# Kernel tuning notes

Measured on AMD Instinct MI355X. Metric: run time of the kernel, lower is better.

## Reference

```python
import jax, jax.numpy as jnp
import numpy as np

D_MODEL = 1024
D_STATE = 16
D_FFN = 4096
D_INNER = 2 * D_MODEL
DT_RANK = D_MODEL // 16  # 64
K = 3  # conv kernel size
B_SZ = 2
L = 2048


def setup_inputs() -> dict:
    key = jax.random.key(0)
    ks = jax.random.split(key, 10)
    f = jnp.float32
    s = 0.02
    A_log = jnp.log(jnp.broadcast_to(jnp.arange(1, D_STATE + 1, dtype=f), (D_INNER, D_STATE)))
    return {
        "x": jax.random.normal(ks[0], (B_SZ, L, D_MODEL), f),
        "in_proj_w": jax.random.normal(ks[1], (2 * D_INNER, D_MODEL), f) * s,
        "conv_w": jax.random.normal(ks[2], (D_INNER, K), f) * s,
        "conv_b": jnp.zeros((D_INNER,), f),
        "x_proj_w": jax.random.normal(ks[3], (DT_RANK + 2 * D_STATE, D_INNER), f) * s,
        "dt_proj_w": jax.random.normal(ks[4], (D_INNER, DT_RANK), f) * s,
        "dt_proj_b": jnp.full((D_INNER,), -4.0, f),  # softplus -> small init dt
        "A_log": A_log,
        "Dp": jnp.ones((D_INNER,), f),
        "out_proj_w": jax.random.normal(ks[5], (D_MODEL, D_INNER), f) * s,
        "w1": jax.random.normal(ks[6], (D_FFN, D_MODEL), f) * s,
        "b1": jnp.zeros((D_FFN,), f),
        "w2": jax.random.normal(ks[7], (D_MODEL, D_FFN), f) * s,
        "b2": jnp.zeros((D_MODEL,), f),
    }


def _mamba(x, in_proj_w, conv_w, conv_b, x_proj_w, dt_proj_w, dt_proj_b, A_log, Dp, out_proj_w):
    # x: [B, L, d_model]
    xz = x @ in_proj_w.T                       # [B, L, 2*d_inner]
    xp, z = jnp.split(xz, 2, axis=-1)          # each [B, L, d_inner]
    # causal depthwise conv over time
    xc = jnp.swapaxes(xp, 1, 2)                # [B, d_inner, L]
    kern = conv_w[:, None, :]                  # [d_inner, 1, K]
    xc = jax.lax.conv_general_dilated(xc, kern, (1,), [(K - 1, 0)], feature_group_count=D_INNER)
    xp = jax.nn.silu(jnp.swapaxes(xc, 1, 2) + conv_b)  # [B, L, d_inner]
    # input-dependent dt, B, C
    dbc = xp @ x_proj_w.T                      # [B, L, dt_rank + 2*d_state]
    dt = jax.nn.softplus(dbc[..., :DT_RANK] @ dt_proj_w.T + dt_proj_b)  # [B, L, d_inner]
    Bm = dbc[..., DT_RANK:DT_RANK + D_STATE]   # [B, L, d_state]
    Cm = dbc[..., DT_RANK + D_STATE:]          # [B, L, d_state]
    A = -jnp.exp(A_log)                        # [d_inner, d_state]

    def step(h, t):
        dt_t, B_t, C_t, x_t = t                # [B,d_inner],[B,n],[B,n],[B,d_inner]
        h = jnp.exp(dt_t[:, :, None] * A) * h + dt_t[:, :, None] * B_t[:, None, :] * x_t[:, :, None]
        y = jnp.einsum('bdn,bn->bd', h, C_t)
        return h, y

    h0 = jnp.zeros((x.shape[0], D_INNER, D_STATE), x.dtype)
    ts = (jnp.swapaxes(dt, 0, 1), jnp.swapaxes(Bm, 0, 1), jnp.swapaxes(Cm, 0, 1), jnp.swapaxes(xp, 0, 1))
    h_final, ys = jax.lax.scan(step, h0, ts)
    y = jnp.swapaxes(ys, 0, 1) + xp * Dp       # [B, L, d_inner]
    y = y * jax.nn.silu(z)
    return y @ out_proj_w.T, h_final


def reference(x, in_proj_w, conv_w, conv_b, x_proj_w, dt_proj_w, dt_proj_b, A_log, Dp, out_proj_w, w1, b1, w2, b2):
    ssm_out, new_state = _mamba(x, in_proj_w, conv_w, conv_b, x_proj_w, dt_proj_w, dt_proj_b, A_log, Dp, out_proj_w)
    x = x + ssm_out
    h = jax.nn.gelu(x @ w1.T + b1, approximate=False)
    x = x + (h @ w2.T + b2)
    return (x, new_state)
```

## Files before the change

### kernel.cpp

```cpp
#include <hip/hip_runtime.h>
#include <hip/hip_bf16.h>
#include <math.h>

using bf16 = __hip_bfloat16;

typedef __attribute__((ext_vector_type(8))) short short8;
typedef __attribute__((ext_vector_type(4))) short shortx4;
typedef __attribute__((ext_vector_type(4))) float floatx4;

#define D_MODEL 1024
#define D_STATE 16
#define D_FFN   4096
#define D_INNER 2048
#define DT_RANK 64
#define BSZ     2
#define SEQ     2048
#define MROWS   (BSZ*SEQ)
#define NCHUNK  16
#define CLEN    (SEQ/NCHUNK)

static __device__ __forceinline__ float bf2f(bf16 v) { return __bfloat162float(v); }
static __device__ __forceinline__ short f2s(float f) {
    bf16 h = __float2bfloat16(f);
    return *reinterpret_cast<short*>(&h);
}
static __device__ __forceinline__ float sbf(short s) {
    union { short s; bf16 h; } u; u.s = s; return __bfloat162float(u.h);
}
static __device__ __forceinline__ float rd(const bf16* p)  { return bf2f(*p); }
static __device__ __forceinline__ float rd(const float* p) { return *p; }
static __device__ __forceinline__ void  wr(bf16* p, float v)  { *p = __float2bfloat16(v); }
static __device__ __forceinline__ void  wr(float* p, float v) { *p = v; }

static __device__ __forceinline__ void gload16(const bf16* g, bf16* l) {
    __builtin_amdgcn_global_load_lds(
        (const __attribute__((address_space(1))) void*)g,
        (__attribute__((address_space(3))) void*)l, 16, 0, 0);
}

#define BK 64

enum { ACT_NONE = 0, ACT_GELU = 1, ACT_SOFTPLUS = 2 };

template<int ACT, bool HAS_BIAS, bool HAS_RES, typename TR, typename TC>
__global__ __launch_bounds__(256)
void gemm_bt(const bf16* __restrict__ A, int lda,
             const bf16* __restrict__ W, int ldw,
             TC* __restrict__ C, int ldc,
             const float* __restrict__ bias,
             const TR* __restrict__ resid, int ldr,
             int K,
             const bf16* __restrict__ W2, TC* __restrict__ C2, int mtiles)
{
    __shared__ __align__(16) bf16 As[128 * BK];
    __shared__ __align__(16) bf16 Bs[128 * BK];

    const int tid  = threadIdx.x;
    const int lane = tid & 63;
    const int wid  = tid >> 6;
    const int wm   = wid >> 1;
    const int wn   = wid & 1;
    const int quad = lane >> 4;
    const int lrow = lane & 15;

    int bx = blockIdx.x, by = blockIdx.y;
    const int gx = gridDim.x;
    if ((gx & 7) == 0) {
        int id = by * gx + bx;
        int bw = gx >> 3;
        int band = id & 7, s = id >> 3;
        bx = band * bw + (s % bw);
        by = s / bw;
    }
    if (by >= mtiles) { by -= mtiles; W = W2; C = C2; }

    const long m0 = (long)by * 128;
    const long n0 = (long)bx * 128;

    const int rsub = lane >> 3;
    const int k8   = (lane & 7) ^ rsub;
    const int g0   = wid * 4;

    const bf16* Ag[4]; const bf16* Wg[4];
    #pragma unroll
    for (int j = 0; j < 4; j++) {
        Ag[j] = A + (m0 + 8 * (g0 + j) + rsub) * (long)lda + k8 * 8;
        Wg[j] = W + (n0 + 8 * (g0 + j) + rsub) * (long)ldw + k8 * 8;
    }

    const int xorl  = lrow & 7;
    const int coK0  = ((quad)     ^ xorl) * 8;
    const int coK1  = ((quad + 4) ^ xorl) * 8;

    floatx4 acc[4][4] = {};

    for (int k0 = 0; k0 < K; k0 += BK) {
        __syncthreads();
        #pragma unroll
        for (int j = 0; j < 4; j++) {
            gload16(Ag[j] + k0, As + (g0 + j) * 512);
            gload16(Wg[j] + k0, Bs + (g0 + j) * 512);
        }
        __syncthreads();

        #pragma unroll
        for (int kk = 0; kk < 2; kk++) {
            const int co = kk ? coK1 : coK0;
            short8 af[4], bfv[4];
            #pragma unroll
            for (int i = 0; i < 4; i++)
                af[i] = *(const short8*)(As + (wm * 64 + i * 16 + lrow) * BK + co);
            #pragma unroll
            for (int j = 0; j < 4; j++)
                bfv[j] = *(const short8*)(Bs + (wn * 64 + j * 16 + lrow) * BK + co);
            #pragma unroll
            for (int i = 0; i < 4; i++)
                #pragma unroll
                for (int j = 0; j < 4; j++)
                    acc[i][j] = __builtin_amdgcn_mfma_f32_16x16x32_bf16(af[i], bfv[j], acc[i][j], 0, 0, 0);
        }
    }

    #pragma unroll
    for (int j = 0; j < 4; j++) {
        const long col = n0 + wn * 64 + j * 16 + lrow;
        float bv = HAS_BIAS ? bias[col] : 0.0f;
        #pragma unroll
        for (int i = 0; i < 4; i++) {
            #pragma unroll
            for (int r = 0; r < 4; r++) {
                const long row = m0 + wm * 64 + i * 16 + quad * 4 + r;
                float v = acc[i][j][r] + bv;
                if (ACT == ACT_GELU)     v = 0.5f * v * (1.0f + erff(v * 0.70710678118f));
                if (ACT == ACT_SOFTPLUS) v = (v > 20.0f) ? v : log1pf(__expf(v));
                if (HAS_RES) v += rd(resid + row * (long)ldr + col);
                wr(C + row * (long)ldc + col, v);
            }
        }
    }
}

__global__ __launch_bounds__(256)
void cvt_bf16(const float* __restrict__ src, bf16* __restrict__ dst)
{
    long i = (long)blockIdx.x * 256 + threadIdx.x;
    float4 a = *((const float4*)src + i * 2);
    float4 b = *((const float4*)src + i * 2 + 1);
    short8 r;
    r[0] = f2s(a.x); r[1] = f2s(a.y); r[2] = f2s(a.z); r[3] = f2s(a.w);
    r[4] = f2s(b.x); r[5] = f2s(b.y); r[6] = f2s(b.z); r[7] = f2s(b.w);
    *(short8*)(dst + i * 8) = r;
}

__global__ __launch_bounds__(256)
void conv_silu(const bf16* __restrict__ xpre, const float* __restrict__ cw,
               const float* __restrict__ cb, bf16* __restrict__ xp)
{
    long i = (long)blockIdx.x * 256 + threadIdx.x;
    int  d  = (int)(i & (D_INNER - 1));
    long bl = i >> 11;
    long l  = bl & (SEQ - 1);

    float w0 = cw[d * 3 + 0];
    float w1 = cw[d * 3 + 1];
    float w2 = cw[d * 3 + 2];
    float acc = cb[d] + w2 * bf2f(xpre[i]);
    if (l >= 1) acc += w1 * bf2f(xpre[i - D_INNER]);
    if (l >= 2) acc += w0 * bf2f(xpre[i - 2 * D_INNER]);
    float s = acc / (1.0f + __expf(-acc));
    xp[i] = __float2bfloat16(s);
}

__global__ __launch_bounds__(256)
void pad_xproj(const float* __restrict__ src, bf16* __restrict__ dst)
{
    int i = blockIdx.x * 256 + threadIdx.x;
    int row = i >> 11, col = i & 2047;
    dst[i] = (row < 96) ? __float2bfloat16(src[row * 2048 + col])
                        : __float2bfloat16(0.0f);
}

#define SROWS 16
#define SDB   64
#define SNB   (CLEN/SROWS)

__global__ __launch_bounds__(256)
void scan_part(const bf16* __restrict__ dt, const bf16* __restrict__ xp,
               const bf16* __restrict__ dbc, const float* __restrict__ Alog,
               float* __restrict__ Pbuf, float* __restrict__ Qbuf)
{
    __shared__ float2 Ap[2][SROWS][SDB];
    __shared__ float  Bp[2][SROWS][16];

    const int tid  = threadIdx.x;
    const int c    = blockIdx.x & (NCHUNK - 1);
    const int dgrp = (blockIdx.x >> 4) & 31;
    const int b    = blockIdx.x >> 9;
    const int d0   = dgrp * SDB;
    const long row0 = (long)b * SEQ + (long)c * CLEN;

    const int sl  = tid >> 4;
    const int sq  = tid & 15;
    const int sd4 = sq * 4;

    const int nt = tid & 3;
    const int dl = tid >> 2;
    const int n0 = nt * 4;
    const int d  = d0 + dl;

    const float4 Av = *(const float4*)(Alog + d * 16 + n0);
    float Ad[4] = { -__expf(Av.x), -__expf(Av.y), -__expf(Av.z), -__expf(Av.w) };

    float rdt[4], rdx[4], rB;
    auto ldb = [&](int bb) {
        long row = row0 + bb * SROWS + sl;
        shortx4 dv = *(const shortx4*)(dt + row * D_INNER + d0 + sd4);
        shortx4 xv = *(const shortx4*)(xp + row * D_INNER + d0 + sd4);
        #pragma unroll
        for (int k = 0; k < 4; k++) {
            float f = sbf(dv[k]);
            rdt[k] = f;
            rdx[k] = f * sbf(xv[k]);
        }
        rB = bf2f(dbc[row * 128 + 64 + sq]);
    };
    auto stb = [&](int bb) {
        int s = bb & 1;
        #pragma unroll
        for (int k = 0; k < 4; k++)
            Ap[s][sl][sd4 + k] = make_float2(rdt[k], rdx[k]);
        Bp[s][sl][sq] = rB;
    };

    float h[4] = {0.f, 0.f, 0.f, 0.f};
    float sdt = 0.f;

    ldb(0); stb(0);
    for (int bb = 0; bb < SNB; bb++) {
        if (bb + 1 < SNB) ldb(bb + 1);
        __syncthreads();
        const int s = bb & 1;
        #pragma unroll
        for (int l = 0; l < SROWS; l++) {
            float2  a  = Ap[s][l][dl];
            floatx4 Bq = *(const floatx4*)&Bp[s][l][n0];
            sdt += a.x;
            #pragma unroll
            for (int k = 0; k < 4; k++)
                h[k] = __expf(a.x * Ad[k]) * h[k] + a.y * Bq[k];
        }
        if (bb + 1 < SNB) stb(bb + 1);
    }

    const long base = ((long)(b * NCHUNK + c) * D_INNER + d) * 16 + n0;
    floatx4 P = { __expf(Ad[0] * sdt), __expf(Ad[1] * sdt),
                  __expf(Ad[2] * sdt), __expf(Ad[3] * sdt) };
    floatx4 Q = { h[0], h[1], h[2], h[3] };
    *(floatx4*)(Pbuf + base) = P;
    *(floatx4*)(Qbuf + base) = Q;
}

__global__ __launch_bounds__(256)
void scan_combine(const float* __restrict__ Pbuf, float* __restrict__ Qbuf,
                  float* __restrict__ state)
{
    long i = (long)blockIdx.x * 256 + threadIdx.x;
    int  n = (int)(i & 15);
    int  d = (int)((i >> 4) & (D_INNER - 1));
    int  b = (int)(i >> 15);
    float h = 0.0f;
    #pragma unroll
    for (int c = 0; c < NCHUNK; c++) {
        const long idx = ((long)(b * NCHUNK + c) * D_INNER + d) * 16 + n;
        float P = Pbuf[idx], Q = Qbuf[idx];
        Qbuf[idx] = h;
        h = P * h + Q;
    }
    state[((long)b * D_INNER + d) * 16 + n] = h;
}

__global__ __launch_bounds__(256)
void scan_final(const bf16* __restrict__ dt, bf16* __restrict__ xp,
                const bf16* __restrict__ dbc, const float* __restrict__ Alog,
                const bf16* __restrict__ z, const float* __restrict__ Dp,
                const float* __restrict__ Qbuf)
{
    __shared__ float2 Ap [2][SROWS][SDB];
    __shared__ float2 BCp[2][SROWS][16];
    __shared__ float2 GWp[2][SROWS][SDB];

    const int tid  = threadIdx.x;
    const int c    = blockIdx.x & (NCHUNK - 1);
    const int dgrp = (blockIdx.x >> 4) & 31;
    const int b    = blockIdx.x >> 9;
    const int d0   = dgrp * SDB;
    const long row0 = (long)b * SEQ + (long)c * CLEN;

    const int sl  = tid >> 4;
    const int sq  = tid & 15;
    const int sd4 = sq * 4;

    const int nt = tid & 3;
    const int dl = tid >> 2;
    const int n0 = nt * 4;
    const int d  = d0 + dl;

    const float4 Av = *(const float4*)(Alog + d * 16 + n0);
    float Ad[4] = { -__expf(Av.x), -__expf(Av.y), -__expf(Av.z), -__expf(Av.w) };
    const float4 Dv = *(const float4*)(Dp + d0 + sd4);
    const float Dk[4] = { Dv.x, Dv.y, Dv.z, Dv.w };

    float rdt[4], rdx[4], rg[4], rw[4], rB, rC;
    auto ldb = [&](int bb) {
        long row = row0 + bb * SROWS + sl;
        shortx4 dv = *(const shortx4*)(dt + row * D_INNER + d0 + sd4);
        shortx4 xv = *(const shortx4*)(xp + row * D_INNER + d0 + sd4);
        shortx4 zv = *(const shortx4*)(z  + row * D_INNER + d0 + sd4);
        #pragma unroll
        for (int k = 0; k < 4; k++) {
            float f  = sbf(dv[k]);
            float xf = sbf(xv[k]);
            float zf = sbf(zv[k]);
            float g  = zf / (1.0f + __expf(-zf));
            rdt[k] = f;
            rdx[k] = f * xf;
            rg[k]  = g;
            rw[k]  = xf * Dk[k] * g;
        }
        rB = bf2f(dbc[row * 128 + 64 + sq]);
        rC = bf2f(dbc[row * 128 + 80 + sq]);
    };
    auto stb = [&](int bb) {
        int s = bb & 1;
        #pragma unroll
        for (int k = 0; k < 4; k++) {
            Ap [s][sl][sd4 + k] = make_float2(rdt[k], rdx[k]);
            GWp[s][sl][sd4 + k] = make_float2(rg[k], rw[k]);
        }
        BCp[s][sl][sq] = make_float2(rB, rC);
    };

    float h[4];
    {
        const long base = ((long)(b * NCHUNK + c) * D_INNER + d) * 16 + n0;
        floatx4 q = *(const floatx4*)(Qbuf + base);
        h[0] = q[0]; h[1] = q[1]; h[2] = q[2]; h[3] = q[3];
    }

    ldb(0); stb(0);
    for (int bb = 0; bb < SNB; bb++) {
        if (bb + 1 < SNB) ldb(bb + 1);
        __syncthreads();
        const int s = bb & 1;
        #pragma unroll
        for (int l = 0; l < SROWS; l++) {
            float2  a   = Ap[s][l][dl];
            floatx4 bc0 = *(const floatx4*)&BCp[s][l][n0];
            floatx4 bc1 = *(const floatx4*)&BCp[s][l][n0 + 2];
            float yv;
            h[0] = __expf(a.x * Ad[0]) * h[0] + a.y * bc0[0];
            yv   = h[0] * bc0[1];
            h[1] = __expf(a.x * Ad[1]) * h[1] + a.y * bc0[2];
            yv  += h[1] * bc0[3];
            h[2] = __expf(a.x * Ad[2]) * h[2] + a.y * bc1[0];
            yv  += h[2] * bc1[1];
            h[3] = __expf(a.x * Ad[3]) * h[3] + a.y * bc1[2];
            yv  += h[3] * bc1[3];
            yv += __shfl_xor(yv, 1);
            yv += __shfl_xor(yv, 2);
            if (nt == 0) {
                float2 gw = GWp[s][l][dl];
                float out = yv * gw.x + gw.y;
                xp[(row0 + bb * SROWS + l) * (long)D_INNER + d0 + dl] =
                    __float2bfloat16(out);
            }
        }
        if (bb + 1 < SNB) stb(bb + 1);
    }
}

extern "C" void kernel_launch(void* const* d_in, const int* in_sizes, int n_in,
                              void* d_out, int out_size, void* d_ws, size_t ws_size,
                              hipStream_t stream)
{
    const float* x      = (const float*)d_in[0];
    const float* inw    = (const float*)d_in[1];
    const float* convw  = (const float*)d_in[2];
    const float* convb  = (const float*)d_in[3];
    const float* xprojw = (const float*)d_in[4];
    const float* dtw    = (const float*)d_in[5];
    const float* dtbias = (const float*)d_in[6];
    const float* Alog   = (const float*)d_in[7];
    const float* Dp     = (const float*)d_in[8];
    const float* outw   = (const float*)d_in[9];
    const float* w1     = (const float*)d_in[10];
    const float* b1     = (const float*)d_in[11];
    const float* w2     = (const float*)d_in[12];
    const float* b2     = (const float*)d_in[13];

    float* out0 = (float*)d_out;
    float* out1 = out0 + (long)MROWS * D_MODEL;

    bf16* buf0 = (bf16*)d_ws;
    bf16* buf1 = buf0 + (long)MROWS * D_INNER;
    bf16* buf2 = buf1 + (long)MROWS * D_INNER;
    bf16* dbc  = buf2 + (long)MROWS * D_INNER;
    bf16* wpad = dbc  + (long)MROWS * 128;
    bf16* W8   = wpad + 128 * 2048;

    float* Pbuf = (float*)d_out;
    float* Qbuf = Pbuf + (long)BSZ * NCHUNK * D_INNER * 16;
    bf16*  xbf  = (bf16*)((char*)d_out + 8 * 1024 * 1024);

    dim3 blk(256);
    const float* nf = nullptr;

    cvt_bf16<<<dim3(2048), blk, 0, stream>>>(x, xbf);
    cvt_bf16<<<dim3(2048), blk, 0, stream>>>(inw, W8);
    pad_xproj<<<dim3(1024), blk, 0, stream>>>(xprojw, wpad);

    gemm_bt<ACT_NONE, false, false, float, bf16>
        <<<dim3(16, 64), blk, 0, stream>>>(
        xbf, D_MODEL, W8, D_MODEL, buf0, D_INNER, nullptr, nf, 0, D_MODEL,
        W8 + (long)D_INNER * D_MODEL, buf2, 32);

    conv_silu<<<dim3(32768), blk, 0, stream>>>(buf0, convw, convb, buf1);

    gemm_bt<ACT_NONE, false, false, float, bf16>
        <<<dim3(1, 32), blk, 0, stream>>>(
        buf1, D_INNER, wpad, D_INNER, dbc, 128, nullptr, nf, 0, D_INNER,
        wpad, dbc, 1000);

    cvt_bf16<<<dim3(64), blk, 0, stream>>>(dtw, W8);
    gemm_bt<ACT_SOFTPLUS, true, false, float, bf16>
        <<<dim3(16, 32), blk, 0, stream>>>(
        dbc, 128, W8, DT_RANK, buf0, D_INNER, dtbias, nf, 0, DT_RANK,
        W8, buf0, 1000);

    scan_part<<<dim3(BSZ * NCHUNK * (D_INNER / SDB)), blk, 0, stream>>>(
        buf0, buf1, dbc, Alog, Pbuf, Qbuf);
    scan_combine<<<dim3(256), blk, 0, stream>>>(Pbuf, Qbuf, out1);
    scan_final<<<dim3(BSZ * NCHUNK * (D_INNER / SDB)), blk, 0, stream>>>(
        buf0, buf1, dbc, Alog, buf2, Dp, Qbuf);

    cvt_bf16<<<dim3(1024), blk, 0, stream>>>(outw, W8);
    gemm_bt<ACT_NONE, false, true, float, bf16>
        <<<dim3(8, 32), blk, 0, stream>>>(
        buf1, D_INNER, W8, D_INNER, buf2, D_MODEL, nullptr, x, D_MODEL, D_INNER,
        W8, buf2, 1000);

    cvt_bf16<<<dim3(2048), blk, 0, stream>>>(w1, W8);
    gemm_bt<ACT_GELU, true, false, float, bf16>
        <<<dim3(32, 32), blk, 0, stream>>>(
        buf2, D_MODEL, W8, D_MODEL, buf0, D_FFN, b1, nf, 0, D_MODEL,
        W8, buf0, 1000);

    cvt_bf16<<<dim3(2048), blk, 0, stream>>>(w2, W8);
    gemm_bt<ACT_NONE, true, true, bf16, float>
        <<<dim3(8, 32), blk, 0, stream>>>(
        buf0, D_FFN, W8, D_FFN, out0, D_MODEL, b2, buf2, D_MODEL, D_FFN,
        W8, out0, 1000);
}
```

Measured before the change: 570.3 us.

## Register-prefetch GEMM with BK=32 and merge weight conversion kernels

The GEMM main loop stops using direct global-to-LDS loads with BK=64. It now prefetches the next K tile into registers while computing the current tile from LDS, with BK=32 and a new XOR swizzle. Separately, the many small fp32-to-bf16 conversion and padding launches are merged into two kernels, and weights go to separate buffers (some aliased into the output region) so the launches are consolidated. The trade is more barriers per K and register pressure against fewer launches and overlap of global loads with MFMA work.

```diff
diff --git a/kernel.cpp b/kernel.cpp
--- a/kernel.cpp
+++ b/kernel.cpp
@@ -32,13 +32,9 @@
 static __device__ __forceinline__ void  wr(bf16* p, float v)  { *p = __float2bfloat16(v); }
 static __device__ __forceinline__ void  wr(float* p, float v) { *p = v; }
 
-static __device__ __forceinline__ void gload16(const bf16* g, bf16* l) {
-    __builtin_amdgcn_global_load_lds(
-        (const __attribute__((address_space(1))) void*)g,
-        (__attribute__((address_space(3))) void*)l, 16, 0, 0);
-}
-
-#define BK 64
+#define WAIT_LGKM0 0xC07F
+
+#define BK 32
 
 enum { ACT_NONE = 0, ACT_GELU = 1, ACT_SOFTPLUS = 2 };
 
@@ -77,48 +73,58 @@
     const long m0 = (long)by * 128;
     const long n0 = (long)bx * 128;
 
-    const int rsub = lane >> 3;
-    const int k8   = (lane & 7) ^ rsub;
-    const int g0   = wid * 4;
-
-    const bf16* Ag[4]; const bf16* Wg[4];
-    #pragma unroll
-    for (int j = 0; j < 4; j++) {
-        Ag[j] = A + (m0 + 8 * (g0 + j) + rsub) * (long)lda + k8 * 8;
-        Wg[j] = W + (n0 + 8 * (g0 + j) + rsub) * (long)ldw + k8 * 8;
-    }
-
-    const int xorl  = lrow & 7;
-    const int coK0  = ((quad)     ^ xorl) * 8;
-    const int coK1  = ((quad + 4) ^ xorl) * 8;
+    const int rlg = lane >> 2;
+    const int kfo = (lane & 3) * 8;
+    const int g0  = wid * 2;
+    const bf16* Ag0 = A + (m0 + (g0 + 0) * 16 + rlg) * (long)lda + kfo;
+    const bf16* Ag1 = A + (m0 + (g0 + 1) * 16 + rlg) * (long)lda + kfo;
+    const bf16* Wg0 = W + (n0 + (g0 + 0) * 16 + rlg) * (long)ldw + kfo;
+    const bf16* Wg1 = W + (n0 + (g0 + 1) * 16 + rlg) * (long)ldw + kfo;
+
+    const int slot = (((lane & 3) ^ ((rlg >> 1) & 3))) * 8;
+    const int so0  = ((g0 + 0) * 16 + rlg) * 32 + slot;
+    const int so1  = ((g0 + 1) * 16 + rlg) * 32 + slot;
+
+    const int co = ((quad ^ ((lrow >> 1) & 3))) * 8;
 
     floatx4 acc[4][4] = {};
 
-    for (int k0 = 0; k0 < K; k0 += BK) {
-        __syncthreads();
-        #pragma unroll
-        for (int j = 0; j < 4; j++) {
-            gload16(Ag[j] + k0, As + (g0 + j) * 512);
-            gload16(Wg[j] + k0, Bs + (g0 + j) * 512);
-        }
-        __syncthreads();
-
-        #pragma unroll
-        for (int kk = 0; kk < 2; kk++) {
-            const int co = kk ? coK1 : coK0;
-            short8 af[4], bfv[4];
-            #pragma unroll
-            for (int i = 0; i < 4; i++)
-                af[i] = *(const short8*)(As + (wm * 64 + i * 16 + lrow) * BK + co);
+    short8 ra0 = *(const short8*)Ag0;
+    short8 ra1 = *(const short8*)Ag1;
+    short8 rb0 = *(const short8*)Wg0;
+    short8 rb1 = *(const short8*)Wg1;
+
+    const int nit = K / BK;
+    for (int it = 0; it < nit; ++it) {
+        *(short8*)(As + so0) = ra0;
+        *(short8*)(As + so1) = ra1;
+        *(short8*)(Bs + so0) = rb0;
+        *(short8*)(Bs + so1) = rb1;
+        __builtin_amdgcn_s_waitcnt(WAIT_LGKM0);
+        __builtin_amdgcn_s_barrier();
+
+        if (it + 1 < nit) {
+            const long ko = (long)(it + 1) * BK;
+            ra0 = *(const short8*)(Ag0 + ko);
+            ra1 = *(const short8*)(Ag1 + ko);
+            rb0 = *(const short8*)(Wg0 + ko);
+            rb1 = *(const short8*)(Wg1 + ko);
+        }
+
+        short8 af[4], bfv[4];
+        #pragma unroll
+        for (int i = 0; i < 4; i++)
+            af[i] = *(const short8*)(As + (wm * 64 + i * 16 + lrow) * BK + co);
+        #pragma unroll
+        for (int j = 0; j < 4; j++)
+            bfv[j] = *(const short8*)(Bs + (wn * 64 + j * 16 + lrow) * BK + co);
+        #pragma unroll
+        for (int i = 0; i < 4; i++)
             #pragma unroll
             for (int j = 0; j < 4; j++)
-                bfv[j] = *(const short8*)(Bs + (wn * 64 + j * 16 + lrow) * BK + co);
-            #pragma unroll
-            for (int i = 0; i < 4; i++)
-                #pragma unroll
-                for (int j = 0; j < 4; j++)
-                    acc[i][j] = __builtin_amdgcn_mfma_f32_16x16x32_bf16(af[i], bfv[j], acc[i][j], 0, 0, 0);
-        }
+                acc[i][j] = __builtin_amdgcn_mfma_f32_16x16x32_bf16(af[i], bfv[j], acc[i][j], 0, 0, 0);
+
+        __builtin_amdgcn_s_barrier();
     }
 
     #pragma unroll
@@ -140,16 +146,54 @@
     }
 }
 
-__global__ __launch_bounds__(256)
-void cvt_bf16(const float* __restrict__ src, bf16* __restrict__ dst)
-{
-    long i = (long)blockIdx.x * 256 + threadIdx.x;
-    float4 a = *((const float4*)src + i * 2);
-    float4 b = *((const float4*)src + i * 2 + 1);
+static __device__ __forceinline__ void cvt8(const float* __restrict__ s,
+                                            bf16* __restrict__ d, long i)
+{
+    float4 a = *((const float4*)s + i * 2);
+    float4 b = *((const float4*)s + i * 2 + 1);
     short8 r;
     r[0] = f2s(a.x); r[1] = f2s(a.y); r[2] = f2s(a.z); r[3] = f2s(a.w);
     r[4] = f2s(b.x); r[5] = f2s(b.y); r[6] = f2s(b.z); r[7] = f2s(b.w);
-    *(short8*)(dst + i * 8) = r;
+    *(short8*)(d + i * 8) = r;
+}
+
+__global__ __launch_bounds__(256)
+void prep1(const float* __restrict__ x, const float* __restrict__ inw,
+           const float* __restrict__ dtw, const float* __restrict__ xprojw,
+           bf16* __restrict__ xbf, bf16* __restrict__ inwb,
+           bf16* __restrict__ dtwb, bf16* __restrict__ wpad)
+{
+    const int bid = blockIdx.x;
+    const long t = threadIdx.x;
+    if (bid < 2048)      cvt8(x,   xbf,  (long)bid * 256 + t);
+    else if (bid < 4096) cvt8(inw, inwb, (long)(bid - 2048) * 256 + t);
+    else if (bid < 4160) cvt8(dtw, dtwb, (long)(bid - 4096) * 256 + t);
+    else {
+        long i = (long)(bid - 4160) * 256 + t;
+        int row = (int)(i >> 8);
+        int c8  = (int)(i & 255) * 8;
+        short8 r = {0, 0, 0, 0, 0, 0, 0, 0};
+        if (row < 96) {
+            const float* s = xprojw + (long)row * 2048 + c8;
+            float4 a = *(const float4*)s, b = *(const float4*)(s + 4);
+            r[0] = f2s(a.x); r[1] = f2s(a.y); r[2] = f2s(a.z); r[3] = f2s(a.w);
+            r[4] = f2s(b.x); r[5] = f2s(b.y); r[6] = f2s(b.z); r[7] = f2s(b.w);
+        }
+        *(short8*)(wpad + (long)row * 2048 + c8) = r;
+    }
+}
+
+__global__ __launch_bounds__(256)
+void prep2(const float* __restrict__ outw, const float* __restrict__ w1,
+           const float* __restrict__ w2,
+           bf16* __restrict__ outwb, bf16* __restrict__ w1b,
+           bf16* __restrict__ w2b)
+{
+    const int bid = blockIdx.x;
+    const long t = threadIdx.x;
+    if (bid < 1024)      cvt8(outw, outwb, (long)bid * 256 + t);
+    else if (bid < 3072) cvt8(w1, w1b, (long)(bid - 1024) * 256 + t);
+    else                 cvt8(w2, w2b, (long)(bid - 3072) * 256 + t);
 }
 
 __global__ __launch_bounds__(256)
@@ -169,15 +213,6 @@
     if (l >= 2) acc += w0 * bf2f(xpre[i - 2 * D_INNER]);
     float s = acc / (1.0f + __expf(-acc));
     xp[i] = __float2bfloat16(s);
-}
-
-__global__ __launch_bounds__(256)
-void pad_xproj(const float* __restrict__ src, bf16* __restrict__ dst)
-{
-    int i = blockIdx.x * 256 + threadIdx.x;
-    int row = i >> 11, col = i & 2047;
-    dst[i] = (row < 96) ? __float2bfloat16(src[row * 2048 + col])
-                        : __float2bfloat16(0.0f);
 }
 
 #define SROWS 16
@@ -408,16 +443,17 @@
     bf16* wpad = dbc  + (long)MROWS * 128;
     bf16* W8   = wpad + 128 * 2048;
 
-    float* Pbuf = (float*)d_out;
-    float* Qbuf = Pbuf + (long)BSZ * NCHUNK * D_INNER * 16;
-    bf16*  xbf  = (bf16*)((char*)d_out + 8 * 1024 * 1024);
+    bf16*  dtwb  = (bf16*)d_out;
+    float* Pbuf  = (float*)d_out;
+    float* Qbuf  = Pbuf + (long)BSZ * NCHUNK * D_INNER * 16;
+    bf16*  xbf   = (bf16*)((char*)d_out + 8 * 1024 * 1024);
+    bf16*  w1b   = (bf16*)d_out;
+    bf16*  outwb = (bf16*)((char*)d_out + 8 * 1024 * 1024);
 
     dim3 blk(256);
     const float* nf = nullptr;
 
-    cvt_bf16<<<dim3(2048), blk, 0, stream>>>(x, xbf);
-    cvt_bf16<<<dim3(2048), blk, 0, stream>>>(inw, W8);
-    pad_xproj<<<dim3(1024), blk, 0, stream>>>(xprojw, wpad);
+    prep1<<<dim3(4288), blk, 0, stream>>>(x, inw, dtw, xprojw, xbf, W8, dtwb, wpad);
 
     gemm_bt<ACT_NONE, false, false, float, bf16>
         <<<dim3(16, 64), blk, 0, stream>>>(
@@ -431,11 +467,10 @@
         buf1, D_INNER, wpad, D_INNER, dbc, 128, nullptr, nf, 0, D_INNER,
         wpad, dbc, 1000);
 
-    cvt_bf16<<<dim3(64), blk, 0, stream>>>(dtw, W8);
     gemm_bt<ACT_SOFTPLUS, true, false, float, bf16>
         <<<dim3(16, 32), blk, 0, stream>>>(
-        dbc, 128, W8, DT_RANK, buf0, D_INNER, dtbias, nf, 0, DT_RANK,
-        W8, buf0, 1000);
+        dbc, 128, dtwb, DT_RANK, buf0, D_INNER, dtbias, nf, 0, DT_RANK,
+        dtwb, buf0, 1000);
 
     scan_part<<<dim3(BSZ * NCHUNK * (D_INNER / SDB)), blk, 0, stream>>>(
         buf0, buf1, dbc, Alog, Pbuf, Qbuf);
@@ -443,19 +478,18 @@
     scan_final<<<dim3(BSZ * NCHUNK * (D_INNER / SDB)), blk, 0, stream>>>(
         buf0, buf1, dbc, Alog, buf2, Dp, Qbuf);
 
-    cvt_bf16<<<dim3(1024), blk, 0, stream>>>(outw, W8);
+    prep2<<<dim3(5120), blk, 0, stream>>>(outw, w1, w2, outwb, w1b, W8);
+
     gemm_bt<ACT_NONE, false, true, float, bf16>
         <<<dim3(8, 32), blk, 0, stream>>>(
-        buf1, D_INNER, W8, D_INNER, buf2, D_MODEL, nullptr, x, D_MODEL, D_INNER,
-        W8, buf2, 1000);
-
-    cvt_bf16<<<dim3(2048), blk, 0, stream>>>(w1, W8);
+        buf1, D_INNER, outwb, D_INNER, buf2, D_MODEL, nullptr, x, D_MODEL, D_INNER,
+        outwb, buf2, 1000);
+
     gemm_bt<ACT_GELU, true, false, float, bf16>
         <<<dim3(32, 32), blk, 0, stream>>>(
-        buf2, D_MODEL, W8, D_MODEL, buf0, D_FFN, b1, nf, 0, D_MODEL,
-        W8, buf0, 1000);
-
-    cvt_bf16<<<dim3(2048), blk, 0, stream>>>(w2, W8);
+        buf2, D_MODEL, w1b, D_MODEL, buf0, D_FFN, b1, nf, 0, D_MODEL,
+        w1b, buf0, 1000);
+
     gemm_bt<ACT_NONE, true, true, bf16, float>
         <<<dim3(8, 32), blk, 0, stream>>>(
         buf0, D_FFN, W8, D_FFN, out0, D_MODEL, b2, buf2, D_MODEL, D_FFN,
```

New measurement: 525.8 us. 1.08x faster.
